# Optimization experiments

Measured on AMD Instinct MI355X. Metric: run time of the kernel, lower is better.

## Reference

```python
import jax, jax.numpy as jnp
import numpy as np

N = 100000      # nodes
E = 3200000     # edges (avg degree 32)
NFEAT = 512
NHID = 256
NCLASS = 40
NLAYERS = 8
T1 = 5
T2 = 5
G1 = 1
G2 = 1
BETA = 0.5      # weight_beta
LAMDA = 0.5
ALPHA = 0.1
EPS = 1e-5


def ortho_trans(weight, T, groups):
    """Newton-Schulz orthogonalization (Ortho_Trans.forward)."""
    g = groups
    Z = weight.reshape(g, weight.shape[0] // g, -1)          # [g, d, k]
    Zc = Z - Z.mean(axis=-1, keepdims=True)
    S = jnp.einsum('gik,gjk->gij', Zc, Zc)                   # covariance [g, d, d]
    eye = jnp.eye(S.shape[-1], dtype=S.dtype)
    S = S + EPS * eye
    norm_S = jnp.sqrt(jnp.sum(S * S, axis=(1, 2), keepdims=True))  # fro norm
    S = S / norm_S
    B0 = jnp.broadcast_to(eye, S.shape)

    def body(B, _):
        B3 = B @ B @ B                                       # matrix_power3
        return 1.5 * B - 0.5 * (B3 @ S), None                # baddbmm(1.5,B,-0.5,B3,S)

    Bt, _ = jax.lax.scan(body, B0, None, length=T)
    W = (Bt @ Zc) / jnp.sqrt(norm_S)
    return W.reshape(weight.shape)


def setup_inputs() -> dict:
    key = jax.random.key(0)
    ks = jax.random.split(key, 8)
    stdv = 1.0 / np.sqrt(NHID)
    return {
        'x': jax.random.normal(ks[0], (N, NFEAT), dtype=jnp.float32),
        'edge_src': jax.random.randint(ks[1], (E,), 0, N, dtype=jnp.int32),
        'edge_dst': jax.random.randint(ks[2], (E,), 0, N, dtype=jnp.int32),
        'edge_weight': jax.random.uniform(ks[3], (E,), dtype=jnp.float32),
        'W0': jax.random.normal(ks[4], (NHID, NFEAT), dtype=jnp.float32) * 0.05,
        'b0': jnp.zeros((NHID,), dtype=jnp.float32),
        'convW': jax.random.uniform(ks[5], (NLAYERS, NHID, NHID), dtype=jnp.float32,
                                    minval=-stdv, maxval=stdv),
        'W1': jax.random.normal(ks[6], (NCLASS, NHID), dtype=jnp.float32) * 0.05,
        'b1': jnp.zeros((NCLASS,), dtype=jnp.float32),
    }


def reference(x, edge_src, edge_dst, edge_weight, W0, b0, convW, W1, b1):
    # fcs[0].weight is orthogonalized at init (Ortho=True)
    W0o = ortho_trans(W0, T1, G1)
    h = jax.nn.relu(x @ W0o.T + b0)                          # [N, NHID]
    h0 = h
    I = jnp.eye(NHID, dtype=h.dtype)
    ls = jnp.arange(1, NLAYERS + 1, dtype=h.dtype)

    def layer(h, inp):
        W, l = inp
        theta = jnp.log(LAMDA / l + 1.0)
        # sparse spmm: hi = adj @ h
        msgs = edge_weight[:, None] * h[edge_src]            # [E, NHID]
        hi = jax.ops.segment_sum(msgs, edge_dst, num_segments=N)
        support = (1.0 - ALPHA) * hi + ALPHA * h0            # variant=False -> r == support
        we = BETA * W + (1.0 - BETA) * I
        t = ortho_trans(we, T2, G2)
        out = jax.nn.relu(theta * (support @ t) + (1.0 - theta) * support)
        return out, None

    h, _ = jax.lax.scan(layer, h, (convW, ls))
    logits = h @ W1.T + b1
    return jax.nn.log_softmax(logits, axis=1)
```

## Files before the change

### kernel.cpp

```cpp
#include <hip/hip_runtime.h>
#include <math.h>

#define NNODES 100000
#define NEDGE  3200000
#define NF     512
#define NH     256
#define NC     40
#define NLAY   8
#define EPSV   1e-5f

#define NBUK 782
#define EPB  16384
#define BCAP 6144

typedef __attribute__((ext_vector_type(8))) short short8;
typedef __attribute__((ext_vector_type(4))) float floatx4;



__device__ __forceinline__ float block_sum_256(float v) {
    __shared__ float sb[8];
    #pragma unroll
    for (int off = 32; off; off >>= 1) v += __shfl_down(v, off, 64);
    if ((threadIdx.x & 63) == 0) sb[threadIdx.x >> 6] = v;
    __syncthreads();
    return sb[0] + sb[1] + sb[2] + sb[3];
}

__device__ __forceinline__ unsigned short bf16_rte(float a) {
    unsigned int u = __float_as_uint(a);
    return (unsigned short)((u + 0x7fffu + ((u >> 16) & 1u)) >> 16);
}
__device__ __forceinline__ unsigned int pack_bf2(float a, float b) {
    unsigned int ua = __float_as_uint(a), ub = __float_as_uint(b);
    ua = (ua + 0x7fffu + ((ua >> 16) & 1u)) >> 16;
    ub = (ub + 0x7fffu + ((ub >> 16) & 1u)) & 0xffff0000u;
    return ua | ub;
}


__global__ __launch_bounds__(1024) void k_histbuk(const int* __restrict__ dst,
                                                  int* __restrict__ bcnt) {
    __shared__ int lh[NBUK];
    const int t = threadIdx.x;
    if (t < NBUK) lh[t] = 0;
    __syncthreads();
    const int e0 = blockIdx.x * EPB;
    #pragma unroll
    for (int i = 0; i < 16; i++) {
        int e = e0 + i * 1024 + t;
        if (e < NEDGE) atomicAdd(&lh[dst[e] >> 7], 1);
    }
    __syncthreads();
    if (t < NBUK) {
        int c = lh[t];
        if (c) atomicAdd(&bcnt[t], c);
    }
}

__global__ __launch_bounds__(1024) void k_scanbuk(const int* __restrict__ bcnt,
                                                  int* __restrict__ bstart,
                                                  int* __restrict__ gcur) {
    __shared__ int s[1024];
    const int t = threadIdx.x;
    int v = (t < NBUK) ? bcnt[t] : 0;
    s[t] = v; __syncthreads();
    for (int off = 1; off < 1024; off <<= 1) {
        int u = (t >= off) ? s[t - off] : 0;
        __syncthreads();
        s[t] += u;
        __syncthreads();
    }
    if (t < NBUK) {
        int e = s[t] - v;
        bstart[t] = e;
        gcur[t] = e;
    }
    if (t == NBUK - 1) bstart[NBUK] = s[t];
}

__global__ __launch_bounds__(1024) void k_binA(const int* __restrict__ src,
                                               const int* __restrict__ dst,
                                               const float* __restrict__ w,
                                               int* __restrict__ gcur,
                                               uint2* __restrict__ gstage) {
    __shared__ int lhist[1024];
    __shared__ int lrun[NBUK];
    __shared__ int lcnt[NBUK];
    const int t = threadIdx.x;
    lhist[t] = 0;
    if (t < NBUK) lcnt[t] = 0;
    __syncthreads();
    const int e0 = blockIdx.x * EPB;
    unsigned int pk[16]; int bk[16]; int dl[16];
    #pragma unroll
    for (int i = 0; i < 16; i++) {
        int e = e0 + i * 1024 + t;
        bk[i] = -1;
        if (e < NEDGE) {
            int d = dst[e];
            bk[i] = d >> 7; dl[i] = d & 127;
            unsigned int wb = bf16_rte(w[e]) & 0x7FFFu;
            pk[i] = ((unsigned int)src[e] << 15) | wb;
            atomicAdd(&lhist[bk[i]], 1);
        }
    }
    __syncthreads();
    if (t < NBUK) {
        int c = lhist[t];
        if (c > 0) lrun[t] = atomicAdd(&gcur[t], c);
    }
    __syncthreads();
    #pragma unroll
    for (int i = 0; i < 16; i++) {
        if (bk[i] >= 0) {
            int p = lrun[bk[i]] + atomicAdd(&lcnt[bk[i]], 1);
            gstage[p] = make_uint2(pk[i], (unsigned int)dl[i]);
        }
    }
}

__global__ __launch_bounds__(256) void k_binB(const int* __restrict__ bstart,
                                              const uint2* __restrict__ gstage,
                                              unsigned int* __restrict__ epack,
                                              int* __restrict__ rstart,
                                              int* __restrict__ counts) {
    __shared__ unsigned int  spk[BCAP];
    __shared__ unsigned char sdl[BCAP];
    __shared__ unsigned int  lout[BCAP];
    __shared__ int lh[256];
    const int b = blockIdx.x, t = threadIdx.x;
    const int base = bstart[b];
    const int end  = bstart[b + 1];
    const int cnt = end - base;
    lh[t] = 0;
    __syncthreads();
    for (int i = t; i < cnt; i += 256) {
        uint2 e = gstage[base + i];
        spk[i] = e.x;
        int d = (int)(e.y & 127u);
        sdl[i] = (unsigned char)d;
        atomicAdd(&lh[d], 1);
    }
    __syncthreads();
    int v = lh[t];
    for (int off = 1; off < 256; off <<= 1) {
        int u = (t >= off) ? lh[t - off] : 0;
        __syncthreads();
        lh[t] += u;
        __syncthreads();
    }
    int excl = lh[t] - v;
    __syncthreads();
    lh[t] = excl;
    if (t < 128) {
        int node = (b << 7) + t;
        if (node < NNODES) { rstart[node] = base + excl; counts[node] = v; }
    }
    __syncthreads();
    for (int i = t; i < cnt; i += 256) {
        int p = atomicAdd(&lh[sdl[i]], 1);
        lout[p] = spk[i];
    }
    __syncthreads();
    for (int i = t; i < cnt; i += 256) epack[base + i] = lout[i];
}


__global__ void k_xbf16(const float* __restrict__ X, unsigned short* __restrict__ Xb, long n8) {
    long i = (long)blockIdx.x * 256 + threadIdx.x;
    if (i >= n8) return;
    const float* p = X + i * 8;
    float4 a = *(const float4*)p;
    float4 b = *(const float4*)(p + 4);
    uint4 o;
    o.x = pack_bf2(a.x, a.y); o.y = pack_bf2(a.z, a.w);
    o.z = pack_bf2(b.x, b.y); o.w = pack_bf2(b.z, b.w);
    *(uint4*)(Xb + i * 8) = o;
}


__global__ void k_zc0(const float* __restrict__ W0, float* __restrict__ Zc0) {
    int r = blockIdx.x, t = threadIdx.x;
    float a = W0[r * NF + t];
    float b = W0[r * NF + 256 + t];
    float mean = block_sum_256(a + b) * (1.0f / 512.0f);
    Zc0[r * NF + t]       = a - mean;
    Zc0[r * NF + 256 + t] = b - mean;
}

__global__ void k_zcC(const float* __restrict__ convW, float* __restrict__ ZcC) {
    int g = blockIdx.x >> 8, r = blockIdx.x & 255, t = threadIdx.x;
    float v = 0.5f * convW[((size_t)g * NH + r) * NH + t] + ((r == t) ? 0.5f : 0.0f);
    float mean = block_sum_256(v) * (1.0f / 256.0f);
    ZcC[((size_t)g * NH + r) * NH + t] = v - mean;
}

__global__ __launch_bounds__(256) void k_gram(const float* __restrict__ Zc0,
                                              const float* __restrict__ ZcC,
                                              float* __restrict__ S) {
    const int b = blockIdx.z;
    const float* A = (b == 0) ? Zc0 : (ZcC + (size_t)(b - 1) * 65536);
    const int K = (b == 0) ? 512 : 256;
    const int r0 = blockIdx.y * 64, c0 = blockIdx.x * 64;
    __shared__ float As[32][76], Bs[32][76];
    const int t = threadIdx.x, tx = t & 15, ty = t >> 4;
    const int lr = t >> 2, lk = (t & 3) * 4;
    float acc[4][4] = {};
    for (int k0 = 0; k0 < K; k0 += 32) {
        float4 a0 = *(const float4*)(A + (size_t)(r0 + lr) * K + k0 + lk);
        float4 a1 = *(const float4*)(A + (size_t)(r0 + lr) * K + k0 + lk + 16);
        As[lk + 0][lr] = a0.x; As[lk + 1][lr] = a0.y; As[lk + 2][lr] = a0.z; As[lk + 3][lr] = a0.w;
        As[lk + 16][lr] = a1.x; As[lk + 17][lr] = a1.y; As[lk + 18][lr] = a1.z; As[lk + 19][lr] = a1.w;
        float4 b0 = *(const float4*)(A + (size_t)(c0 + lr) * K + k0 + lk);
        float4 b1 = *(const float4*)(A + (size_t)(c0 + lr) * K + k0 + lk + 16);
        Bs[lk + 0][lr] = b0.x; Bs[lk + 1][lr] = b0.y; Bs[lk + 2][lr] = b0.z; Bs[lk + 3][lr] = b0.w;
        Bs[lk + 16][lr] = b1.x; Bs[lk + 17][lr] = b1.y; Bs[lk + 18][lr] = b1.z; Bs[lk + 19][lr] = b1.w;
        __syncthreads();
        #pragma unroll
        for (int kk = 0; kk < 32; kk++) {
            float a[4], bb[4];
            *(float4*)&a[0]  = *(const float4*)&As[kk][ty * 4];
            *(float4*)&bb[0] = *(const float4*)&Bs[kk][tx * 4];
            #pragma unroll
            for (int i = 0; i < 4; i++)
                #pragma unroll
                for (int j = 0; j < 4; j++) acc[i][j] = fmaf(a[i], bb[j], acc[i][j]);
        }
        __syncthreads();
    }
    #pragma unroll
    for (int i = 0; i < 4; i++)
        #pragma unroll
        for (int j = 0; j < 4; j++) {
            int r = r0 + ty * 4 + i, c = c0 + tx * 4 + j;
            float v = acc[i][j];
            if (r == c) v += EPSV;
            S[(size_t)b * 65536 + r * NH + c] = v;
        }
}

__global__ void k_fro(const float* __restrict__ S, float* __restrict__ scales) {
    __shared__ float sb[8];
    const int b = blockIdx.x, t = threadIdx.x;
    const float* p = S + (size_t)b * 65536;
    float s = 0.f;
    for (int i = t; i < 65536; i += 256) { float v = p[i]; s = fmaf(v, v, s); }
    #pragma unroll
    for (int off = 32; off; off >>= 1) s += __shfl_down(s, off, 64);
    if ((t & 63) == 0) sb[t >> 6] = s;
    __syncthreads();
    if (t == 0) {
        float nrm = sqrtf(sb[0] + sb[1] + sb[2] + sb[3]);
        scales[b]      = 1.0f / nrm;
        scales[16 + b] = rsqrtf(nrm);
    }
}

__global__ void k_initB1(const float* __restrict__ S, const float* __restrict__ scales,
                         float* __restrict__ B) {
    int i = blockIdx.x * 256 + threadIdx.x;
    int b = i >> 16, m = i & 65535;
    float v = -0.5f * scales[b] * S[i];
    if ((m >> 8) == (m & 255)) v += 1.5f;
    B[i] = v;
}

__global__ __launch_bounds__(256) void k_ns_pair(const float* __restrict__ Bb,
                                                 const float* __restrict__ Smat,
                                                 float* __restrict__ T1b,
                                                 float* __restrict__ T2b) {
    const int b = blockIdx.z;
    const int bb = (b < 9) ? b : b - 9;
    const float* A  = Bb + (size_t)bb * 65536;
    const float* Bm = (b < 9) ? A : (Smat + (size_t)bb * 65536);
    float* C = (b < 9) ? (T1b + (size_t)bb * 65536) : (T2b + (size_t)bb * 65536);
    const int r0 = blockIdx.y * 64, c0 = blockIdx.x * 64;
    __shared__ float As[32][76], Bs[32][76];
    const int t = threadIdx.x, tx = t & 15, ty = t >> 4;
    const int lr = t >> 2, lk = (t & 3) * 4;
    const int bk = t >> 3, bc = (t & 7) * 8;
    float acc[4][4] = {};
    for (int k0 = 0; k0 < 256; k0 += 32) {
        float4 a0 = *(const float4*)(A + (size_t)(r0 + lr) * 256 + k0 + lk);
        float4 a1 = *(const float4*)(A + (size_t)(r0 + lr) * 256 + k0 + lk + 16);
        As[lk + 0][lr] = a0.x; As[lk + 1][lr] = a0.y; As[lk + 2][lr] = a0.z; As[lk + 3][lr] = a0.w;
        As[lk + 16][lr] = a1.x; As[lk + 17][lr] = a1.y; As[lk + 18][lr] = a1.z; As[lk + 19][lr] = a1.w;
        float4 b0 = *(const float4*)(Bm + (size_t)(k0 + bk) * 256 + c0 + bc);
        float4 b1 = *(const float4*)(Bm + (size_t)(k0 + bk) * 256 + c0 + bc + 4);
        *(float4*)&Bs[bk][bc]     = b0;
        *(float4*)&Bs[bk][bc + 4] = b1;
        __syncthreads();
        #pragma unroll
        for (int kk = 0; kk < 32; kk++) {
            float a[4], bb2[4];
            *(float4*)&a[0]   = *(const float4*)&As[kk][ty * 4];
            *(float4*)&bb2[0] = *(const float4*)&Bs[kk][tx * 4];
            #pragma unroll
            for (int i = 0; i < 4; i++)
                #pragma unroll
                for (int j = 0; j < 4; j++) acc[i][j] = fmaf(a[i], bb2[j], acc[i][j]);
        }
        __syncthreads();
    }
    #pragma unroll
    for (int i = 0; i < 4; i++)
        #pragma unroll
        for (int j = 0; j < 4; j++)
            C[(size_t)(r0 + ty * 4 + i) * 256 + c0 + tx * 4 + j] = acc[i][j];
}

__global__ __launch_bounds__(256) void k_small_nn(const float* __restrict__ A0,
                                                  const float* __restrict__ B0,
                                                  float* __restrict__ C0,
                                                  int sA, int sB, int sC,
                                                  int K, int Ncols, int mode,
                                                  const float* __restrict__ scale) {
    const int b = blockIdx.z;
    const float* A = A0 + (size_t)b * sA;
    const float* Bm = B0 + (size_t)b * sB;
    float* C = C0 + (size_t)b * sC;
    const int r0 = blockIdx.y * 64, c0 = blockIdx.x * 64;
    __shared__ float As[32][76], Bs[32][76];
    const int t = threadIdx.x, tx = t & 15, ty = t >> 4;
    const int lr = t >> 2, lk = (t & 3) * 4;
    const int bk = t >> 3, bc = (t & 7) * 8;
    float acc[4][4] = {};
    for (int k0 = 0; k0 < K; k0 += 32) {
        float4 a0 = *(const float4*)(A + (size_t)(r0 + lr) * K + k0 + lk);
        float4 a1 = *(const float4*)(A + (size_t)(r0 + lr) * K + k0 + lk + 16);
        As[lk + 0][lr] = a0.x; As[lk + 1][lr] = a0.y; As[lk + 2][lr] = a0.z; As[lk + 3][lr] = a0.w;
        As[lk + 16][lr] = a1.x; As[lk + 17][lr] = a1.y; As[lk + 18][lr] = a1.z; As[lk + 19][lr] = a1.w;
        float4 b0 = *(const float4*)(Bm + (size_t)(k0 + bk) * Ncols + c0 + bc);
        float4 b1 = *(const float4*)(Bm + (size_t)(k0 + bk) * Ncols + c0 + bc + 4);
        *(float4*)&Bs[bk][bc]     = b0;
        *(float4*)&Bs[bk][bc + 4] = b1;
        __syncthreads();
        #pragma unroll
        for (int kk = 0; kk < 32; kk++) {
            float a[4], bb[4];
            *(float4*)&a[0]  = *(const float4*)&As[kk][ty * 4];
            *(float4*)&bb[0] = *(const float4*)&Bs[kk][tx * 4];
            #pragma unroll
            for (int i = 0; i < 4; i++)
                #pragma unroll
                for (int j = 0; j < 4; j++) acc[i][j] = fmaf(a[i], bb[j], acc[i][j]);
        }
        __syncthreads();
    }
    #pragma unroll
    for (int i = 0; i < 4; i++)
        #pragma unroll
        for (int j = 0; j < 4; j++) {
            size_t idx = (size_t)(r0 + ty * 4 + i) * Ncols + c0 + tx * 4 + j;
            if (mode == 1) C[idx] = 1.5f * C[idx] - 0.5f * scale[b] * acc[i][j];
            else C[idx] = scale[b] * acc[i][j];
        }
}


__global__ void k_prepM(const float* __restrict__ tbuf, unsigned short* __restrict__ Mpack) {
    int idx = blockIdx.x * 256 + threadIdx.x;
    int lane = idx & 63;
    int tg   = (idx >> 6) & 15;
    int s    = (idx >> 10) & 1;
    int c    = (idx >> 11) & 3;
    int l    = idx >> 13;
    float theta = logf(0.5f / (float)(l + 1) + 1.0f);
    float mtheta = 1.0f - theta;
    int n  = tg * 16 + (lane & 15);
    int k0 = c * 64 + s * 32 + (lane >> 4) * 8;
    const float* T = tbuf + (size_t)l * 65536;
    unsigned short o[8];
    #pragma unroll
    for (int j = 0; j < 8; j++) {
        int kp = k0 + j;
        int kn = (kp & 0xC0) | ((kp & 3) << 4) | ((kp >> 2) & 15);
        float v = theta * T[(size_t)kn * 256 + n] + ((kn == n) ? mtheta : 0.0f);
        o[j] = bf16_rte(v);
    }
    *(uint4*)(Mpack + (size_t)idx * 8) = *(uint4*)o;
}

__global__ void k_prepW0(const float* __restrict__ W0o, unsigned short* __restrict__ Wpack) {
    int idx = blockIdx.x * 256 + threadIdx.x;
    int lane = idx & 63;
    int tg   = (idx >> 6) & 15;
    int s    = (idx >> 10) & 1;
    int c    = idx >> 11;
    int n  = tg * 16 + (lane & 15);
    int k0 = c * 64 + s * 32 + (lane >> 4) * 8;
    const float* p = W0o + (size_t)n * NF + k0;
    unsigned short o[8];
    #pragma unroll
    for (int j = 0; j < 8; j++) o[j] = bf16_rte(p[j]);
    *(uint4*)(Wpack + (size_t)idx * 8) = *(uint4*)o;
}


__global__ __launch_bounds__(256) void k_fc0_mfma(const unsigned short* __restrict__ Xb,
                                                  const unsigned short* __restrict__ Wp,
                                                  const float* __restrict__ bias,
                                                  unsigned char* __restrict__ h0u8,
                                                  float* __restrict__ h0scale) {
    __shared__ int rmax[64];
    const int t = threadIdx.x, lane = t & 63, w = t >> 6;
    const int q = lane >> 4, m = lane & 15;
    const int r0 = blockIdx.x * 64;
    if (t < 64) rmax[t] = 0;
    floatx4 acc[4][4] = {};
    #pragma unroll
    for (int c = 0; c < 8; c++) {
        #pragma unroll
        for (int s = 0; s < 2; s++) {
            short8 afr[4];
            #pragma unroll
            for (int i = 0; i < 4; i++) {
                int row = r0 + i * 16 + m; if (row > NNODES - 1) row = NNODES - 1;
                afr[i] = *(const short8*)(Xb + (size_t)row * NF + c * 64 + s * 32 + q * 8);
            }
            #pragma unroll
            for (int tg = 0; tg < 4; tg++) {
                short8 bfr = *(const short8*)(Wp + (size_t)c * 16384 + s * 8192
                                              + (w * 4 + tg) * 512 + lane * 8);
                #pragma unroll
                for (int i = 0; i < 4; i++)
                    acc[i][tg] = __builtin_amdgcn_mfma_f32_16x16x32_bf16(afr[i], bfr, acc[i][tg], 0, 0, 0);
            }
        }
    }
    #pragma unroll
    for (int tg = 0; tg < 4; tg++) {
        float bv = bias[w * 64 + tg * 16 + m];
        #pragma unroll
        for (int i = 0; i < 4; i++)
            #pragma unroll
            for (int r = 0; r < 4; r++)
                acc[i][tg][r] = fmaxf(acc[i][tg][r] + bv, 0.f);
    }
    __syncthreads();
    #pragma unroll
    for (int i = 0; i < 4; i++)
        #pragma unroll
        for (int r = 0; r < 4; r++) {
            float mx = fmaxf(fmaxf(acc[i][0][r], acc[i][1][r]),
                             fmaxf(acc[i][2][r], acc[i][3][r]));
            mx = fmaxf(mx, __shfl_xor(mx, 1));
            mx = fmaxf(mx, __shfl_xor(mx, 2));
            mx = fmaxf(mx, __shfl_xor(mx, 4));
            mx = fmaxf(mx, __shfl_xor(mx, 8));
            if (m == 0) atomicMax(&rmax[i * 16 + q * 4 + r], __float_as_int(mx));
        }
    __syncthreads();
    #pragma unroll
    for (int i = 0; i < 4; i++)
        #pragma unroll
        for (int r = 0; r < 4; r++) {
            int row = r0 + i * 16 + q * 4 + r;
            if (row >= NNODES) continue;
            float rm = __int_as_float(rmax[i * 16 + q * 4 + r]);
            float qs = rm > 0.f ? 255.0f / rm : 0.f;
            unsigned int b0 = (unsigned int)fmaf(acc[i][0][r], qs, 0.5f);
            unsigned int b1 = (unsigned int)fmaf(acc[i][1][r], qs, 0.5f);
            unsigned int b2 = (unsigned int)fmaf(acc[i][2][r], qs, 0.5f);
            unsigned int b3 = (unsigned int)fmaf(acc[i][3][r], qs, 0.5f);
            *(unsigned int*)(h0u8 + (size_t)row * NH + w * 64 + m * 4) =
                b0 | (b1 << 8) | (b2 << 16) | (b3 << 24);
        }
    if (t < 64 && r0 + t < NNODES)
        h0scale[r0 + t] = __int_as_float(rmax[t]) * (1.0f / 255.0f);
}


__global__ __launch_bounds__(256) void k_spmm(const int* __restrict__ rstart,
                                              const int* __restrict__ counts,
                                              const unsigned int* __restrict__ epack,
                                              const unsigned char* __restrict__ hu8,
                                              const float* __restrict__ hscale,
                                              const unsigned char* __restrict__ h0u8,
                                              const float* __restrict__ h0scale,
                                              unsigned short* __restrict__ supbf) {
    __shared__ int2 se[4][64];
    const int wv = threadIdx.x >> 6, lane = threadIdx.x & 63;
    const int node = blockIdx.x * 4 + wv;
    const int start = rstart[node], deg = counts[node];
    float a0 = 0.f, a1 = 0.f, a2 = 0.f, a3 = 0.f;
    for (int base = 0; base < deg; base += 64) {
        int j = base + lane;
        if (j < deg) {
            unsigned int u = epack[start + j];
            int s = (int)(u >> 15);
            float wt = __uint_as_float((u & 0x7FFFu) << 16);
            se[wv][lane] = make_int2(s, __float_as_int(wt * hscale[s] * 0.9f));
        }
        int mm = deg - base; if (mm > 64) mm = 64;
        int e = 0;
        for (; e + 8 <= mm; e += 8) {
            float ww[8]; unsigned int g[8];
            #pragma unroll
            for (int u = 0; u < 8; u++) {
                int2 ed = se[wv][e + u];
                ww[u] = __int_as_float(ed.y);
                g[u] = *(const unsigned int*)(hu8 + ((size_t)ed.x << 8) + (lane << 2));
            }
            #pragma unroll
            for (int u = 0; u < 8; u++) {
                a0 = fmaf(ww[u], (float)(g[u] & 0xFFu), a0);
                a1 = fmaf(ww[u], (float)((g[u] >> 8) & 0xFFu), a1);
                a2 = fmaf(ww[u], (float)((g[u] >> 16) & 0xFFu), a2);
                a3 = fmaf(ww[u], (float)(g[u] >> 24), a3);
            }
        }
        for (; e < mm; e++) {
            int2 ed = se[wv][e];
            float ww = __int_as_float(ed.y);
            unsigned int g = *(const unsigned int*)(hu8 + ((size_t)ed.x << 8) + (lane << 2));
            a0 = fmaf(ww, (float)(g & 0xFFu), a0);
            a1 = fmaf(ww, (float)((g >> 8) & 0xFFu), a1);
            a2 = fmaf(ww, (float)((g >> 16) & 0xFFu), a2);
            a3 = fmaf(ww, (float)(g >> 24), a3);
        }
    }
    unsigned int rg = *(const unsigned int*)(h0u8 + ((size_t)node << 8) + (lane << 2));
    float rs = h0scale[node] * 0.1f;
    float o0 = fmaf(rs, (float)(rg & 0xFFu), a0);
    float o1 = fmaf(rs, (float)((rg >> 8) & 0xFFu), a1);
    float o2 = fmaf(rs, (float)((rg >> 16) & 0xFFu), a2);
    float o3 = fmaf(rs, (float)(rg >> 24), a3);
    uint2 ov;
    ov.x = pack_bf2(o0, o1);
    ov.y = pack_bf2(o2, o3);
    *(uint2*)(supbf + ((size_t)node << 8) + (lane << 2)) = ov;
}


__global__ __launch_bounds__(256) void k_gemm_layer(const unsigned short* __restrict__ Sbf,
                                                    const unsigned short* __restrict__ Mp,
                                                    unsigned char* __restrict__ out_u8,
                                                    float* __restrict__ out_scale,
                                                    unsigned short* __restrict__ out_bf) {
    __shared__ int rmax[64];
    const int t = threadIdx.x, lane = t & 63, w = t >> 6;
    const int q = lane >> 4, m = lane & 15;
    const int r0 = blockIdx.x * 64;
    if (t < 64) rmax[t] = 0;
    floatx4 acc[4][4] = {};
    #pragma unroll
    for (int c = 0; c < 4; c++) {
        #pragma unroll
        for (int s = 0; s < 2; s++) {
            short8 afr[4];
            #pragma unroll
            for (int i = 0; i < 4; i++) {
                int row = r0 + i * 16 + m; if (row > NNODES - 1) row = NNODES - 1;
                afr[i] = *(const short8*)(Sbf + (size_t)row * NH + c * 64 + s * 32 + q * 8);
            }
            #pragma unroll
            for (int tg = 0; tg < 4; tg++) {
                short8 bfr = *(const short8*)(Mp + (size_t)c * 16384 + s * 8192
                                              + (w * 4 + tg) * 512 + lane * 8);
                #pragma unroll
                for (int i = 0; i < 4; i++)
                    acc[i][tg] = __builtin_amdgcn_mfma_f32_16x16x32_bf16(afr[i], bfr, acc[i][tg], 0, 0, 0);
            }
        }
    }
    #pragma unroll
    for (int i = 0; i < 4; i++)
        #pragma unroll
        for (int tg = 0; tg < 4; tg++)
            #pragma unroll
            for (int r = 0; r < 4; r++)
                acc[i][tg][r] = fmaxf(acc[i][tg][r], 0.f);

    if (out_bf) {
        #pragma unroll
        for (int i = 0; i < 4; i++)
            #pragma unroll
            for (int tg = 0; tg < 4; tg++) {
                int col = w * 64 + tg * 16 + m;
                #pragma unroll
                for (int r = 0; r < 4; r++) {
                    int row = r0 + i * 16 + q * 4 + r;
                    if (row >= NNODES) continue;
                    out_bf[(size_t)row * NH + col] = bf16_rte(acc[i][tg][r]);
                }
            }
        return;
    }
    __syncthreads();
    #pragma unroll
    for (int i = 0; i < 4; i++)
        #pragma unroll
        for (int r = 0; r < 4; r++) {
            float mx = fmaxf(fmaxf(acc[i][0][r], acc[i][1][r]),
                             fmaxf(acc[i][2][r], acc[i][3][r]));
            mx = fmaxf(mx, __shfl_xor(mx, 1));
            mx = fmaxf(mx, __shfl_xor(mx, 2));
            mx = fmaxf(mx, __shfl_xor(mx, 4));
            mx = fmaxf(mx, __shfl_xor(mx, 8));
            if (m == 0) atomicMax(&rmax[i * 16 + q * 4 + r], __float_as_int(mx));
        }
    __syncthreads();
    #pragma unroll
    for (int i = 0; i < 4; i++)
        #pragma unroll
        for (int r = 0; r < 4; r++) {
            int row = r0 + i * 16 + q * 4 + r;
            if (row >= NNODES) continue;
            float rm = __int_as_float(rmax[i * 16 + q * 4 + r]);
            float qs = rm > 0.f ? 255.0f / rm : 0.f;
            unsigned int b0 = (unsigned int)fmaf(acc[i][0][r], qs, 0.5f);
            unsigned int b1 = (unsigned int)fmaf(acc[i][1][r], qs, 0.5f);
            unsigned int b2 = (unsigned int)fmaf(acc[i][2][r], qs, 0.5f);
            unsigned int b3 = (unsigned int)fmaf(acc[i][3][r], qs, 0.5f);
            *(unsigned int*)(out_u8 + (size_t)row * NH + w * 64 + m * 4) =
                b0 | (b1 << 8) | (b2 << 16) | (b3 << 24);
        }
    if (t < 64 && r0 + t < NNODES)
        out_scale[r0 + t] = __int_as_float(rmax[t]) * (1.0f / 255.0f);
}


__global__ __launch_bounds__(256) void k_logits(const unsigned short* __restrict__ hb,
                                                const float* __restrict__ W1,
                                                const float* __restrict__ b1,
                                                float* __restrict__ out, int nrows) {
    __shared__ float hs[32][260];
    __shared__ float Ws[40][260];
    __shared__ float ls[32][44];
    __shared__ float lse[32];
    const int t = threadIdx.x;
    const int row0 = blockIdx.x * 32;
    for (int i = t; i < 40 * 64; i += 256) {
        int c = i >> 6, k4 = i & 63;
        *(float4*)&Ws[c][k4 * 4] = *(const float4*)(W1 + (size_t)c * NH + k4 * 4);
    }
    for (int i = t; i < 32 * 32; i += 256) {
        int r = i >> 5, k8 = i & 31;
        int gr = row0 + r;
        uint4 v = make_uint4(0u, 0u, 0u, 0u);
        if (gr < nrows) v = *(const uint4*)(hb + ((size_t)gr << 8) + k8 * 8);
        float* d = &hs[r][k8 * 8];
        d[0] = __uint_as_float(v.x << 16); d[1] = __uint_as_float(v.x & 0xffff0000u);
        d[2] = __uint_as_float(v.y << 16); d[3] = __uint_as_float(v.y & 0xffff0000u);
        d[4] = __uint_as_float(v.z << 16); d[5] = __uint_as_float(v.z & 0xffff0000u);
        d[6] = __uint_as_float(v.w << 16); d[7] = __uint_as_float(v.w & 0xffff0000u);
    }
    __syncthreads();
    const int r = t & 31, cg = t >> 5;
    float acc[5];
    #pragma unroll
    for (int j = 0; j < 5; j++) acc[j] = b1[cg * 5 + j];
    for (int k = 0; k < NH; k++) {
        float hv = hs[r][k];
        #pragma unroll
        for (int j = 0; j < 5; j++) acc[j] = fmaf(hv, Ws[cg * 5 + j][k], acc[j]);
    }
    #pragma unroll
    for (int j = 0; j < 5; j++) ls[r][cg * 5 + j] = acc[j];
    __syncthreads();
    if (t < 32) {
        float m = -3.4e38f;
        for (int c = 0; c < NC; c++) m = fmaxf(m, ls[t][c]);
        float s = 0.f;
        for (int c = 0; c < NC; c++) s += expf(ls[t][c] - m);
        lse[t] = m + logf(s);
    }
    __syncthreads();
    for (int i = t; i < 32 * NC; i += 256) {
        int r2 = i / NC, c = i % NC;
        int gr = row0 + r2;
        if (gr < nrows) out[(size_t)gr * NC + c] = ls[r2][c] - lse[r2];
    }
}


extern "C" void kernel_launch(void* const* d_in, const int* in_sizes, int n_in,
                              void* d_out, int out_size, void* d_ws, size_t ws_size,
                              hipStream_t stream) {
    const float* x      = (const float*)d_in[0];
    const int*   e_src  = (const int*)d_in[1];
    const int*   e_dst  = (const int*)d_in[2];
    const float* e_w    = (const float*)d_in[3];
    const float* W0     = (const float*)d_in[4];
    const float* b0     = (const float*)d_in[5];
    const float* convW  = (const float*)d_in[6];
    const float* W1     = (const float*)d_in[7];
    const float* b1     = (const float*)d_in[8];
    float* out = (float*)d_out;

    char* ws = (char*)d_ws;
    const size_t OFF_H0U8   = 0;
    const size_t OFF_HU8A   = OFF_H0U8 + (size_t)NNODES * NH;
    const size_t OFF_HU8B   = OFF_HU8A + (size_t)NNODES * NH;
    const size_t OFF_H0SC   = OFF_HU8B + (size_t)NNODES * NH;
    const size_t OFF_SCA    = OFF_H0SC + (size_t)NNODES * 4;
    const size_t OFF_SCB    = OFF_SCA + (size_t)NNODES * 4;
    const size_t OFF_SUPBF  = OFF_SCB + (size_t)NNODES * 4;
    const size_t OFF_HBF    = OFF_SUPBF + (size_t)NNODES * NH * 2;
    const size_t OFF_XBF    = OFF_HBF + (size_t)NNODES * NH * 2;
    const size_t OFF_EPACK  = OFF_XBF + (size_t)NNODES * NF * 2;
    const size_t OFF_RSTART = OFF_EPACK + (size_t)NEDGE * 4;
    const size_t OFF_COUNTS = OFF_RSTART + (size_t)NNODES * 4;
    const size_t OFF_CURSOR = OFF_COUNTS + (size_t)NNODES * 4;
    const size_t OFF_BSUM   = OFF_CURSOR + (size_t)NNODES * 4;
    const size_t OFF_ZC0    = OFF_BSUM + 1024;
    const size_t OFF_ZCC    = OFF_ZC0 + 256 * 512 * 4;
    const size_t OFF_S      = OFF_ZCC + 8 * 65536 * 4;
    const size_t OFF_B      = OFF_S + 9 * 65536 * 4;
    const size_t OFF_T1     = OFF_B + 9 * 65536 * 4;
    const size_t OFF_T2     = OFF_T1 + 9 * 65536 * 4;
    const size_t OFF_T      = OFF_T2 + 9 * 65536 * 4;
    const size_t OFF_W0O    = OFF_T + 8 * 65536 * 4;
    const size_t OFF_SCALES = OFF_W0O + 256 * 512 * 4;
    const size_t OFF_MPACK  = OFF_SCALES + 1024;
    const size_t OFF_WPACK  = OFF_MPACK + 8 * 65536 * 2;

    unsigned char* h0u8 = (unsigned char*)(ws + OFF_H0U8);
    unsigned char* hu8A = (unsigned char*)(ws + OFF_HU8A);
    unsigned char* hu8B = (unsigned char*)(ws + OFF_HU8B);
    float* h0sc = (float*)(ws + OFF_H0SC);
    float* scA  = (float*)(ws + OFF_SCA);
    float* scB  = (float*)(ws + OFF_SCB);
    unsigned short* supbf = (unsigned short*)(ws + OFF_SUPBF);
    unsigned short* hbf   = (unsigned short*)(ws + OFF_HBF);
    unsigned short* xbf   = (unsigned short*)(ws + OFF_XBF);
    unsigned int* epack  = (unsigned int*)(ws + OFF_EPACK);
    int*    rstart = (int*)(ws + OFF_RSTART);
    int*    counts = (int*)(ws + OFF_COUNTS);
    int*    gcur   = (int*)(ws + OFF_CURSOR);
    int*    bcnt   = (int*)(ws + OFF_CURSOR + 4096);
    int*    bstart = (int*)(ws + OFF_CURSOR + 8192);
    float*  Zc0    = (float*)(ws + OFF_ZC0);
    float*  ZcC    = (float*)(ws + OFF_ZCC);
    float*  Smat   = (float*)(ws + OFF_S);
    float*  Bb     = (float*)(ws + OFF_B);
    float*  T1b    = (float*)(ws + OFF_T1);
    float*  T2b    = (float*)(ws + OFF_T2);
    float*  tbuf   = (float*)(ws + OFF_T);
    float*  W0o    = (float*)(ws + OFF_W0O);
    float*  scales = (float*)(ws + OFF_SCALES);
    unsigned short* Mpack = (unsigned short*)(ws + OFF_MPACK);
    unsigned short* Wpack = (unsigned short*)(ws + OFF_WPACK);
    uint2* gstage = (uint2*)(ws + OFF_SUPBF);

    (void)in_sizes; (void)n_in; (void)out_size; (void)ws_size;

    hipMemsetAsync(bcnt, 0, (size_t)NBUK * 4, stream);
    const int NBA = (NEDGE + EPB - 1) / EPB;
    k_histbuk<<<NBA, 1024, 0, stream>>>(e_dst, bcnt);
    k_scanbuk<<<1, 1024, 0, stream>>>(bcnt, bstart, gcur);
    k_binA<<<NBA, 1024, 0, stream>>>(e_src, e_dst, e_w, gcur, gstage);
    k_binB<<<NBUK, 256, 0, stream>>>(bstart, gstage, epack, rstart, counts);

    const long N8 = (long)NNODES * NF / 8;
    k_xbf16<<<(int)((N8 + 255) / 256), 256, 0, stream>>>(x, xbf, N8);

    k_zc0<<<256, 256, 0, stream>>>(W0, Zc0);
    k_zcC<<<8 * 256, 256, 0, stream>>>(convW, ZcC);
    k_gram<<<dim3(4, 4, 9), 256, 0, stream>>>(Zc0, ZcC, Smat);
    k_fro<<<9, 256, 0, stream>>>(Smat, scales);
    k_initB1<<<9 * 256, 256, 0, stream>>>(Smat, scales, Bb);
    for (int it = 1; it < 5; it++) {
        k_ns_pair<<<dim3(4, 4, 18), 256, 0, stream>>>(Bb, Smat, T1b, T2b);
        k_small_nn<<<dim3(4, 4, 9), 256, 0, stream>>>(T1b, T2b, Bb, 65536, 65536, 65536,
                                                      256, 256, 1, scales);
    }
    k_small_nn<<<dim3(8, 4, 1), 256, 0, stream>>>(Bb, Zc0, W0o, 0, 0, 0,
                                                  256, 512, 2, scales + 16);
    k_small_nn<<<dim3(4, 4, 8), 256, 0, stream>>>(Bb + 65536, ZcC, tbuf, 65536, 65536, 65536,
                                                  256, 256, 2, scales + 17);

    k_prepM<<<256, 256, 0, stream>>>(tbuf, Mpack);
    k_prepW0<<<64, 256, 0, stream>>>(W0o, Wpack);

    const int GB = (NNODES + 63) / 64;
    k_fc0_mfma<<<GB, 256, 0, stream>>>(xbf, Wpack, b0, h0u8, h0sc);

    const unsigned char* hin = h0u8;
    const float* hinsc = h0sc;
    unsigned char* u8bufs[2] = { hu8A, hu8B };
    float* scbufs[2] = { scA, scB };
    for (int l = 1; l <= NLAY; l++) {
        k_spmm<<<NNODES / 4, 256, 0, stream>>>(rstart, counts, epack, hin, hinsc,
                                               h0u8, h0sc, supbf);
        const unsigned short* Mp = Mpack + (size_t)(l - 1) * 65536;
        if (l == NLAY) {
            k_gemm_layer<<<GB, 256, 0, stream>>>(supbf, Mp, nullptr, nullptr, hbf);
        } else {
            unsigned char* ou = u8bufs[(l - 1) & 1];
            float* os = scbufs[(l - 1) & 1];
            k_gemm_layer<<<GB, 256, 0, stream>>>(supbf, Mp, ou, os, nullptr);
            hin = ou; hinsc = os;
        }
    }

    k_logits<<<(NNODES + 31) / 32, 256, 0, stream>>>(hbf, W1, b1, out, NNODES);
}
```

Measured before the change: 2.215 ms.

## Fuse SpMM aggregation and per-layer GEMM into one kernel via LDS tile

Merges the gather-based SpMM and the MFMA layer GEMM into a single kernel. Each block aggregates 64 nodes into a swizzled bf16 tile in shared memory, then runs the GEMM directly from LDS. This removes the global round trip of the support matrix and one launch per layer. In exchange the block uses 32KB+ of LDS, which lowers occupancy for the latency-bound gather phase. It also runs fewer, larger blocks (1563 instead of 25000), with each wave handling 16 nodes in sequence.

New measurement: 2.896 ms. 30.7% more time.

```diff
diff --git a/kernel.cpp b/kernel.cpp
--- a/kernel.cpp
+++ b/kernel.cpp
@@ -471,79 +471,81 @@
         h0scale[r0 + t] = __int_as_float(rmax[t]) * (1.0f / 255.0f);
 }
 
-
-__global__ __launch_bounds__(256) void k_spmm(const int* __restrict__ rstart,
-                                              const int* __restrict__ counts,
-                                              const unsigned int* __restrict__ epack,
-                                              const unsigned char* __restrict__ hu8,
-                                              const float* __restrict__ hscale,
-                                              const unsigned char* __restrict__ h0u8,
-                                              const float* __restrict__ h0scale,
-                                              unsigned short* __restrict__ supbf) {
+__global__ __launch_bounds__(256) void k_layer(const int* __restrict__ rstart,
+                                               const int* __restrict__ counts,
+                                               const unsigned int* __restrict__ epack,
+                                               const unsigned char* __restrict__ hu8,
+                                               const float* __restrict__ hscale,
+                                               const unsigned char* __restrict__ h0u8,
+                                               const float* __restrict__ h0scale,
+                                               const unsigned short* __restrict__ Mp,
+                                               unsigned char* __restrict__ out_u8,
+                                               float* __restrict__ out_scale,
+                                               unsigned short* __restrict__ out_bf) {
+    __shared__ unsigned char sup[64 * 512];
     __shared__ int2 se[4][64];
-    const int wv = threadIdx.x >> 6, lane = threadIdx.x & 63;
-    const int node = blockIdx.x * 4 + wv;
-    const int start = rstart[node], deg = counts[node];
-    float a0 = 0.f, a1 = 0.f, a2 = 0.f, a3 = 0.f;
-    for (int base = 0; base < deg; base += 64) {
-        int j = base + lane;
-        if (j < deg) {
-            unsigned int u = epack[start + j];
-            int s = (int)(u >> 15);
-            float wt = __uint_as_float((u & 0x7FFFu) << 16);
-            se[wv][lane] = make_int2(s, __float_as_int(wt * hscale[s] * 0.9f));
-        }
-        int mm = deg - base; if (mm > 64) mm = 64;
-        int e = 0;
-        for (; e + 8 <= mm; e += 8) {
-            float ww[8]; unsigned int g[8];
-            #pragma unroll
-            for (int u = 0; u < 8; u++) {
-                int2 ed = se[wv][e + u];
-                ww[u] = __int_as_float(ed.y);
-                g[u] = *(const unsigned int*)(hu8 + ((size_t)ed.x << 8) + (lane << 2));
-            }
-            #pragma unroll
-            for (int u = 0; u < 8; u++) {
-                a0 = fmaf(ww[u], (float)(g[u] & 0xFFu), a0);
-                a1 = fmaf(ww[u], (float)((g[u] >> 8) & 0xFFu), a1);
-                a2 = fmaf(ww[u], (float)((g[u] >> 16) & 0xFFu), a2);
-                a3 = fmaf(ww[u], (float)(g[u] >> 24), a3);
-            }
-        }
-        for (; e < mm; e++) {
-            int2 ed = se[wv][e];
-            float ww = __int_as_float(ed.y);
-            unsigned int g = *(const unsigned int*)(hu8 + ((size_t)ed.x << 8) + (lane << 2));
-            a0 = fmaf(ww, (float)(g & 0xFFu), a0);
-            a1 = fmaf(ww, (float)((g >> 8) & 0xFFu), a1);
-            a2 = fmaf(ww, (float)((g >> 16) & 0xFFu), a2);
-            a3 = fmaf(ww, (float)(g >> 24), a3);
-        }
-    }
-    unsigned int rg = *(const unsigned int*)(h0u8 + ((size_t)node << 8) + (lane << 2));
-    float rs = h0scale[node] * 0.1f;
-    float o0 = fmaf(rs, (float)(rg & 0xFFu), a0);
-    float o1 = fmaf(rs, (float)((rg >> 8) & 0xFFu), a1);
-    float o2 = fmaf(rs, (float)((rg >> 16) & 0xFFu), a2);
-    float o3 = fmaf(rs, (float)(rg >> 24), a3);
-    uint2 ov;
-    ov.x = pack_bf2(o0, o1);
-    ov.y = pack_bf2(o2, o3);
-    *(uint2*)(supbf + ((size_t)node << 8) + (lane << 2)) = ov;
-}
-
-
-__global__ __launch_bounds__(256) void k_gemm_layer(const unsigned short* __restrict__ Sbf,
-                                                    const unsigned short* __restrict__ Mp,
-                                                    unsigned char* __restrict__ out_u8,
-                                                    float* __restrict__ out_scale,
-                                                    unsigned short* __restrict__ out_bf) {
     __shared__ int rmax[64];
     const int t = threadIdx.x, lane = t & 63, w = t >> 6;
-    const int q = lane >> 4, m = lane & 15;
     const int r0 = blockIdx.x * 64;
     if (t < 64) rmax[t] = 0;
+
+    for (int nl0 = 0; nl0 < 16; nl0++) {
+        const int nl = w * 16 + nl0;
+        const int node = r0 + nl;
+        float o0 = 0.f, o1 = 0.f, o2 = 0.f, o3 = 0.f;
+        if (node < NNODES) {
+            const int start = rstart[node], deg = counts[node];
+            for (int base = 0; base < deg; base += 64) {
+                int j = base + lane;
+                if (j < deg) {
+                    unsigned int u = epack[start + j];
+                    int s = (int)(u >> 15);
+                    float wt = __uint_as_float((u & 0x7FFFu) << 16);
+                    se[w][lane] = make_int2(s, __float_as_int(wt * hscale[s] * 0.9f));
+                }
+                int mm = deg - base; if (mm > 64) mm = 64;
+                int e = 0;
+                for (; e + 8 <= mm; e += 8) {
+                    float ww[8]; unsigned int g[8];
+                    #pragma unroll
+                    for (int u2 = 0; u2 < 8; u2++) {
+                        int2 ed = se[w][e + u2];
+                        ww[u2] = __int_as_float(ed.y);
+                        g[u2] = *(const unsigned int*)(hu8 + ((size_t)ed.x << 8) + (lane << 2));
+                    }
+                    #pragma unroll
+                    for (int u2 = 0; u2 < 8; u2++) {
+                        o0 = fmaf(ww[u2], (float)(g[u2] & 0xFFu), o0);
+                        o1 = fmaf(ww[u2], (float)((g[u2] >> 8) & 0xFFu), o1);
+                        o2 = fmaf(ww[u2], (float)((g[u2] >> 16) & 0xFFu), o2);
+                        o3 = fmaf(ww[u2], (float)(g[u2] >> 24), o3);
+                    }
+                }
+                for (; e < mm; e++) {
+                    int2 ed = se[w][e];
+                    float ww = __int_as_float(ed.y);
+                    unsigned int g = *(const unsigned int*)(hu8 + ((size_t)ed.x << 8) + (lane << 2));
+                    o0 = fmaf(ww, (float)(g & 0xFFu), o0);
+                    o1 = fmaf(ww, (float)((g >> 8) & 0xFFu), o1);
+                    o2 = fmaf(ww, (float)((g >> 16) & 0xFFu), o2);
+                    o3 = fmaf(ww, (float)(g >> 24), o3);
+                }
+            }
+            unsigned int rg = *(const unsigned int*)(h0u8 + ((size_t)node << 8) + (lane << 2));
+            float rs = h0scale[node] * 0.1f;
+            o0 = fmaf(rs, (float)(rg & 0xFFu), o0);
+            o1 = fmaf(rs, (float)((rg >> 8) & 0xFFu), o1);
+            o2 = fmaf(rs, (float)((rg >> 16) & 0xFFu), o2);
+            o3 = fmaf(rs, (float)(rg >> 24), o3);
+        }
+        uint2 ov;
+        ov.x = pack_bf2(o0, o1);
+        ov.y = pack_bf2(o2, o3);
+        *(uint2*)&sup[nl * 512 + ((lane * 8) ^ ((nl & 7) << 4))] = ov;
+    }
+    __syncthreads();
+
+    const int q = lane >> 4, m = lane & 15;
     floatx4 acc[4][4] = {};
     #pragma unroll
     for (int c = 0; c < 4; c++) {
@@ -552,8 +554,9 @@
             short8 afr[4];
             #pragma unroll
             for (int i = 0; i < 4; i++) {
-                int row = r0 + i * 16 + m; if (row > NNODES - 1) row = NNODES - 1;
-                afr[i] = *(const short8*)(Sbf + (size_t)row * NH + c * 64 + s * 32 + q * 8);
+                int rl = i * 16 + m;
+                afr[i] = *(const short8*)&sup[rl * 512
+                           + ((c * 128 + s * 64 + q * 16) ^ ((rl & 7) << 4))];
             }
             #pragma unroll
             for (int tg = 0; tg < 4; tg++) {
@@ -588,7 +591,6 @@
             }
         return;
     }
-    __syncthreads();
     #pragma unroll
     for (int i = 0; i < 4; i++)
         #pragma unroll
@@ -723,7 +725,6 @@
     float* h0sc = (float*)(ws + OFF_H0SC);
     float* scA  = (float*)(ws + OFF_SCA);
     float* scB  = (float*)(ws + OFF_SCB);
-    unsigned short* supbf = (unsigned short*)(ws + OFF_SUPBF);
     unsigned short* hbf   = (unsigned short*)(ws + OFF_HBF);
     unsigned short* xbf   = (unsigned short*)(ws + OFF_XBF);
     unsigned int* epack  = (unsigned int*)(ws + OFF_EPACK);
@@ -783,15 +784,15 @@
     unsigned char* u8bufs[2] = { hu8A, hu8B };
     float* scbufs[2] = { scA, scB };
     for (int l = 1; l <= NLAY; l++) {
-        k_spmm<<<NNODES / 4, 256, 0, stream>>>(rstart, counts, epack, hin, hinsc,
-                                               h0u8, h0sc, supbf);
         const unsigned short* Mp = Mpack + (size_t)(l - 1) * 65536;
         if (l == NLAY) {
-            k_gemm_layer<<<GB, 256, 0, stream>>>(supbf, Mp, nullptr, nullptr, hbf);
+            k_layer<<<GB, 256, 0, stream>>>(rstart, counts, epack, hin, hinsc,
+                                            h0u8, h0sc, Mp, nullptr, nullptr, hbf);
         } else {
             unsigned char* ou = u8bufs[(l - 1) & 1];
             float* os = scbufs[(l - 1) & 1];
-            k_gemm_layer<<<GB, 256, 0, stream>>>(supbf, Mp, ou, os, nullptr);
+            k_layer<<<GB, 256, 0, stream>>>(rstart, counts, epack, hin, hinsc,
+                                            h0u8, h0sc, Mp, ou, os, nullptr);
             hin = ou; hinsc = os;
         }
     }
```
